# Kernel tuning notes

Hardware: AMD Instinct MI355X
Metric: run time of the kernel (lower is better)

The kernel has to match this reference:

```python
import jax, jax.numpy as jnp
import numpy as np

B, N, E = 128, 2000, 2000
EMBED, HIDDEN = 256, 512


def setup_inputs() -> dict:
    key = jax.random.key(0)
    k1, k2, k3, k4, k5, k6, k7 = jax.random.split(key, 7)
    node_embeddings = jax.random.normal(k1, (B, N, EMBED), dtype=jnp.float32)
    locs = jax.random.uniform(k2, (B, N, 2), dtype=jnp.float32)
    edge_list = jax.random.randint(k3, (B, E, 2), 0, N, dtype=jnp.int64)
    in_dim = 2 * EMBED + 1
    # Kaiming-ish init for the two Linear layers of edge_scorer
    W1 = jax.random.normal(k4, (in_dim, HIDDEN), dtype=jnp.float32) / np.sqrt(in_dim)
    b1 = jnp.zeros((HIDDEN,), dtype=jnp.float32)
    W2 = jax.random.normal(k5, (HIDDEN, 1), dtype=jnp.float32) / np.sqrt(HIDDEN)
    b2 = jnp.zeros((1,), dtype=jnp.float32)
    return {
        "node_embeddings": node_embeddings,
        "locs": locs,
        "edge_list": edge_list,
        "delete_bias": 0,
        "W1": W1,
        "b1": b1,
        "W2": W2,
        "b2": b2,
    }


def reference(node_embeddings, locs, edge_list, delete_bias, W1, b1, W2, b2):
    # valid mask for -1-padded edges
    valid = (edge_list[..., 0] >= 0) & (edge_list[..., 1] >= 0)  # (B, E)
    edges = jnp.clip(edge_list, 0, None)
    bidx = jnp.arange(node_embeddings.shape[0])[:, None]  # (B, 1)
    i, j = edges[..., 0], edges[..., 1]  # (B, E)
    emb_i = node_embeddings[bidx, i]  # (B, E, D)
    emb_j = node_embeddings[bidx, j]  # (B, E, D)
    d = locs[bidx, i] - locs[bidx, j]  # (B, E, 2)
    dist = jnp.sqrt(jnp.sum(d * d, axis=-1, keepdims=True))  # (B, E, 1)
    feats = jnp.concatenate([emb_i, emb_j, dist], axis=-1)  # (B, E, 2D+1)
    h = jax.nn.relu(jnp.einsum('bef,fh->beh', feats, W1) + b1)
    logits = (jnp.einsum('beh,ho->beo', h, W2) + b2)[..., 0]  # (B, E)
    logits = jnp.where(valid, logits, -jnp.inf)
    return logits + jnp.float32(delete_bias)
```

## Files before the change

### kernel.cpp

```cpp
#include <hip/hip_runtime.h>
#include <math.h>

#define EMBED    256
#define HIDDEN   512
#define KDIM     512
#define Nn       2000
#define Ee       2000
#define BM       64
#define NTHREADS 512
#define NBLK     4000
#define PITCH    72

typedef __attribute__((ext_vector_type(8)))  short bf16x8;
typedef __attribute__((ext_vector_type(16))) float f32x16;

static __device__ __forceinline__ short f2bf(float f) {
  unsigned u = __builtin_bit_cast(unsigned, f);
  u += 0x7fffu + ((u >> 16) & 1u);
  return (short)(u >> 16);
}

static __device__ __forceinline__ bf16x8 cvt8(float4 a, float4 b) {
  bf16x8 v;
  v[0]=f2bf(a.x); v[1]=f2bf(a.y); v[2]=f2bf(a.z); v[3]=f2bf(a.w);
  v[4]=f2bf(b.x); v[5]=f2bf(b.y); v[6]=f2bf(b.z); v[7]=f2bf(b.w);
  return v;
}

__global__ void w1f_kernel(const float* __restrict__ W1, short* __restrict__ W1F) {
  const int t  = blockIdx.x * 512 + threadIdx.x;
  const int l  = t & 63;
  const int tk = (t >> 6) & 31;
  const int tn = t >> 11;
  const int n  = tn * 32 + (l & 31);
  const int k0 = tk * 16 + (l >> 5) * 8;
  bf16x8 v;
#pragma unroll
  for (int q = 0; q < 8; ++q)
    v[q] = f2bf(W1[(size_t)(k0 + q) * HIDDEN + n]);
  *(bf16x8*)(W1F + (size_t)t * 8) = v;
}

__global__ __launch_bounds__(NTHREADS, 4)
void edge_kernel(const float* __restrict__ emb, const float* __restrict__ locs,
                 const int* __restrict__ edges, const int* __restrict__ dbias,
                 const float* __restrict__ W1, const float* __restrict__ b1,
                 const float* __restrict__ W2, const float* __restrict__ b2,
                 const short* __restrict__ W1F, float* __restrict__ out)
{
  __shared__ short  feat[2][BM][PITCH];
  __shared__ float4 ep_s[HIDDEN];
  __shared__ float  part_s[8][BM];
  __shared__ float  dist_s[BM];
  __shared__ int    valid_s[BM];
  __shared__ int    ibase_s[BM];
  __shared__ int    jbase_s[BM];

  const int tid = threadIdx.x;

  const int wg = (blockIdx.x & 7) * (NBLK / 8) + (blockIdx.x >> 3);

  if (tid < BM) {
    const int g  = wg * BM + tid;
    const int b  = g / Ee;
    const int i0 = edges[2 * g];
    const int j0 = edges[2 * g + 1];
    valid_s[tid] = (i0 >= 0) && (j0 >= 0);
    const int ib = b * Nn + (i0 < 0 ? 0 : i0);
    const int jb = b * Nn + (j0 < 0 ? 0 : j0);
    ibase_s[tid] = ib;
    jbase_s[tid] = jb;
    const float dx = locs[2 * (size_t)ib]     - locs[2 * (size_t)jb];
    const float dy = locs[2 * (size_t)ib + 1] - locs[2 * (size_t)jb + 1];
    dist_s[tid] = sqrtf(dx * dx + dy * dy);
  }
  ep_s[tid] = make_float4(b1[tid], W1[(size_t)KDIM * HIDDEN + tid], W2[tid], 0.f);
  asm volatile("s_waitcnt lgkmcnt(0)" ::: "memory");
  __builtin_amdgcn_s_barrier();
  asm volatile("" ::: "memory");

  const int e  = tid >> 3;
  const int sq = tid & 7;

  const int lane = tid & 63;
  const int ng   = tid >> 6;
  const int ln31 = lane & 31;
  const int kg   = lane >> 5;

  {
    const float* p = emb + (size_t)ibase_s[e] * EMBED + sq * 8;
    float4 v0 = *(const float4*)(p);
    float4 v1 = *(const float4*)(p + 4);
    *(bf16x8*)&feat[0][e][sq * 8] = cvt8(v0, v1);
  }
  float4 gh0, gh1;
  {
    const float* p = emb + (size_t)ibase_s[e] * EMBED + 64 + sq * 8;
    gh0 = *(const float4*)(p);
    gh1 = *(const float4*)(p + 4);
  }
  asm volatile("s_waitcnt lgkmcnt(0)" ::: "memory");
  __builtin_amdgcn_s_barrier();
  asm volatile("" ::: "memory");

  f32x16 acc[2][2];
#pragma unroll
  for (int et = 0; et < 2; ++et)
#pragma unroll
    for (int nt = 0; nt < 2; ++nt)
#pragma unroll
      for (int q = 0; q < 16; ++q) acc[et][nt][q] = 0.f;

#pragma unroll 1
  for (int c = 0; c < 8; ++c) {
    const int bb = c & 1;
    const int nb = bb ^ 1;

    const short* wb = W1F + ((size_t)(ng * 2) * 32 + c * 4) * 512 + lane * 8;
    bf16x8 wa0[4], wa1[4];
#pragma unroll
    for (int ks = 0; ks < 4; ++ks) {
      wa0[ks] = *(const bf16x8*)(wb + ks * 512);
      wa1[ks] = *(const bf16x8*)(wb + 32 * 512 + ks * 512);
    }
#pragma unroll
    for (int ks = 0; ks < 4; ++ks) {
      bf16x8 fb0 = *(const bf16x8*)(&feat[bb][ln31][ks * 16 + kg * 8]);
      bf16x8 fb1 = *(const bf16x8*)(&feat[bb][32 + ln31][ks * 16 + kg * 8]);
      acc[0][0] = __builtin_amdgcn_mfma_f32_32x32x16_bf16(wa0[ks], fb0, acc[0][0], 0, 0, 0);
      acc[0][1] = __builtin_amdgcn_mfma_f32_32x32x16_bf16(wa1[ks], fb0, acc[0][1], 0, 0, 0);
      acc[1][0] = __builtin_amdgcn_mfma_f32_32x32x16_bf16(wa0[ks], fb1, acc[1][0], 0, 0, 0);
      acc[1][1] = __builtin_amdgcn_mfma_f32_32x32x16_bf16(wa1[ks], fb1, acc[1][1], 0, 0, 0);
    }

    if (c < 7)
      *(bf16x8*)&feat[nb][e][sq * 8] = cvt8(gh0, gh1);

    __builtin_amdgcn_sched_barrier(0);
    if (c < 6) {
      const int cc = c + 2;
      const int rb = (cc < 4) ? ibase_s[e] : jbase_s[e];
      const float* p = emb + (size_t)rb * EMBED + (cc & 3) * 64 + sq * 8;
      gh0 = *(const float4*)(p);
      gh1 = *(const float4*)(p + 4);
    }
    __builtin_amdgcn_sched_barrier(0);

    asm volatile("s_waitcnt lgkmcnt(0)" ::: "memory");
    __builtin_amdgcn_s_barrier();
    asm volatile("" ::: "memory");
  }

  const float d0 = dist_s[ln31];
  const float d1 = dist_s[32 + ln31];
  float ps0 = 0.f, ps1 = 0.f;
#pragma unroll
  for (int nt = 0; nt < 2; ++nt) {
#pragma unroll
    for (int r = 0; r < 16; ++r) {
      const int n = ng * 64 + nt * 32 + (r & 3) + ((r >> 2) << 3) + (kg << 2);
      const float4 ep = ep_s[n];
      float p0 = acc[0][nt][r] + ep.x + d0 * ep.y;
      float p1 = acc[1][nt][r] + ep.x + d1 * ep.y;
      ps0 += fmaxf(p0, 0.f) * ep.z;
      ps1 += fmaxf(p1, 0.f) * ep.z;
    }
  }
  ps0 += __shfl_xor(ps0, 32, 64);
  ps1 += __shfl_xor(ps1, 32, 64);
  if (lane < 32) {
    part_s[ng][ln31]      = ps0;
    part_s[ng][32 + ln31] = ps1;
  }
  __syncthreads();

  if (tid < BM) {
    float s = 0.f;
#pragma unroll
    for (int w = 0; w < 8; ++w) s += part_s[w][tid];
    float logit = s + b2[0] + (float)dbias[0];
    if (!valid_s[tid]) logit = -__builtin_inff();
    out[(size_t)wg * BM + tid] = logit;
  }
}

extern "C" void kernel_launch(void* const* d_in, const int* in_sizes, int n_in,
                              void* d_out, int out_size, void* d_ws, size_t ws_size,
                              hipStream_t stream) {
  const float* emb   = (const float*)d_in[0];
  const float* locs  = (const float*)d_in[1];
  const int*   edges = (const int*)d_in[2];
  const int*   dbias = (const int*)d_in[3];
  const float* W1    = (const float*)d_in[4];
  const float* b1    = (const float*)d_in[5];
  const float* W2    = (const float*)d_in[6];
  const float* b2    = (const float*)d_in[7];
  float*       out   = (float*)d_out;
  short*       W1F   = (short*)d_ws;

  w1f_kernel<<<dim3(64), dim3(512), 0, stream>>>(W1, W1F);
  edge_kernel<<<dim3(NBLK), dim3(NTHREADS), 0, stream>>>(
      emb, locs, edges, dbias, W1, b1, W2, b2, (const short*)W1F, out);
}
```

Measured before the change: 164.7 us.

## Double edge tile to 128 per block and prefetch W1 fragments across chunks

```diff
diff --git a/kernel.cpp b/kernel.cpp
--- a/kernel.cpp
+++ b/kernel.cpp
@@ -6,9 +6,9 @@
 #define KDIM     512
 #define Nn       2000
 #define Ee       2000
-#define BM       64
+#define BM       128
 #define NTHREADS 512
-#define NBLK     4000
+#define NBLK     2000
 #define PITCH    72
 
 typedef __attribute__((ext_vector_type(8)))  short bf16x8;
@@ -41,7 +41,7 @@
   *(bf16x8*)(W1F + (size_t)t * 8) = v;
 }
 
-__global__ __launch_bounds__(NTHREADS, 4)
+__global__ __launch_bounds__(NTHREADS, 2)
 void edge_kernel(const float* __restrict__ emb, const float* __restrict__ locs,
                  const int* __restrict__ edges, const int* __restrict__ dbias,
                  const float* __restrict__ W1, const float* __restrict__ b1,
@@ -79,8 +79,8 @@
   __builtin_amdgcn_s_barrier();
   asm volatile("" ::: "memory");
 
-  const int e  = tid >> 3;
-  const int sq = tid & 7;
+  const int e  = tid >> 2;
+  const int sq = tid & 3;
 
   const int lane = tid & 63;
   const int ng   = tid >> 6;
@@ -88,24 +88,38 @@
   const int kg   = lane >> 5;
 
   {
-    const float* p = emb + (size_t)ibase_s[e] * EMBED + sq * 8;
+    const float* p = emb + (size_t)ibase_s[e] * EMBED + sq * 16;
     float4 v0 = *(const float4*)(p);
     float4 v1 = *(const float4*)(p + 4);
-    *(bf16x8*)&feat[0][e][sq * 8] = cvt8(v0, v1);
-  }
-  float4 gh0, gh1;
+    float4 v2 = *(const float4*)(p + 8);
+    float4 v3 = *(const float4*)(p + 12);
+    *(bf16x8*)&feat[0][e][sq * 16]     = cvt8(v0, v1);
+    *(bf16x8*)&feat[0][e][sq * 16 + 8] = cvt8(v2, v3);
+  }
+  bf16x8 wc0[4], wc1[4];
   {
-    const float* p = emb + (size_t)ibase_s[e] * EMBED + 64 + sq * 8;
-    gh0 = *(const float4*)(p);
-    gh1 = *(const float4*)(p + 4);
+    const short* wb = W1F + (size_t)(ng * 64) * 512 + lane * 8;
+#pragma unroll
+    for (int ks = 0; ks < 4; ++ks) {
+      wc0[ks] = *(const bf16x8*)(wb + ks * 512);
+      wc1[ks] = *(const bf16x8*)(wb + 32 * 512 + ks * 512);
+    }
+  }
+  float4 g0, g1, g2, g3;
+  {
+    const float* p = emb + (size_t)ibase_s[e] * EMBED + 64 + sq * 16;
+    g0 = *(const float4*)(p);
+    g1 = *(const float4*)(p + 4);
+    g2 = *(const float4*)(p + 8);
+    g3 = *(const float4*)(p + 12);
   }
   asm volatile("s_waitcnt lgkmcnt(0)" ::: "memory");
   __builtin_amdgcn_s_barrier();
   asm volatile("" ::: "memory");
 
-  f32x16 acc[2][2];
-#pragma unroll
-  for (int et = 0; et < 2; ++et)
+  f32x16 acc[4][2];
+#pragma unroll
+  for (int et = 0; et < 4; ++et)
 #pragma unroll
     for (int nt = 0; nt < 2; ++nt)
 #pragma unroll
@@ -114,63 +128,77 @@
 #pragma unroll 1
   for (int c = 0; c < 8; ++c) {
     const int bb = c & 1;
-    const int nb = bb ^ 1;
-
-    const short* wb = W1F + ((size_t)(ng * 2) * 32 + c * 4) * 512 + lane * 8;
-    bf16x8 wa0[4], wa1[4];
+    const int nbuf = bb ^ 1;
+
+    bf16x8 wn0[4], wn1[4];
+    if (c < 7) {
+      const short* wb = W1F + (size_t)(ng * 64 + (c + 1) * 4) * 512 + lane * 8;
+#pragma unroll
+      for (int ks = 0; ks < 4; ++ks) {
+        wn0[ks] = *(const bf16x8*)(wb + ks * 512);
+        wn1[ks] = *(const bf16x8*)(wb + 32 * 512 + ks * 512);
+      }
+    }
+
 #pragma unroll
     for (int ks = 0; ks < 4; ++ks) {
-      wa0[ks] = *(const bf16x8*)(wb + ks * 512);
-      wa1[ks] = *(const bf16x8*)(wb + 32 * 512 + ks * 512);
-    }
-#pragma unroll
-    for (int ks = 0; ks < 4; ++ks) {
-      bf16x8 fb0 = *(const bf16x8*)(&feat[bb][ln31][ks * 16 + kg * 8]);
-      bf16x8 fb1 = *(const bf16x8*)(&feat[bb][32 + ln31][ks * 16 + kg * 8]);
-      acc[0][0] = __builtin_amdgcn_mfma_f32_32x32x16_bf16(wa0[ks], fb0, acc[0][0], 0, 0, 0);
-      acc[0][1] = __builtin_amdgcn_mfma_f32_32x32x16_bf16(wa1[ks], fb0, acc[0][1], 0, 0, 0);
-      acc[1][0] = __builtin_amdgcn_mfma_f32_32x32x16_bf16(wa0[ks], fb1, acc[1][0], 0, 0, 0);
-      acc[1][1] = __builtin_amdgcn_mfma_f32_32x32x16_bf16(wa1[ks], fb1, acc[1][1], 0, 0, 0);
-    }
-
-    if (c < 7)
-      *(bf16x8*)&feat[nb][e][sq * 8] = cvt8(gh0, gh1);
+#pragma unroll
+      for (int et = 0; et < 4; ++et) {
+        bf16x8 fb = *(const bf16x8*)(&feat[bb][et * 32 + ln31][ks * 16 + kg * 8]);
+        acc[et][0] = __builtin_amdgcn_mfma_f32_32x32x16_bf16(wc0[ks], fb, acc[et][0], 0, 0, 0);
+        acc[et][1] = __builtin_amdgcn_mfma_f32_32x32x16_bf16(wc1[ks], fb, acc[et][1], 0, 0, 0);
+      }
+    }
+
+    if (c < 7) {
+      *(bf16x8*)&feat[nbuf][e][sq * 16]     = cvt8(g0, g1);
+      *(bf16x8*)&feat[nbuf][e][sq * 16 + 8] = cvt8(g2, g3);
+    }
 
     __builtin_amdgcn_sched_barrier(0);
     if (c < 6) {
       const int cc = c + 2;
       const int rb = (cc < 4) ? ibase_s[e] : jbase_s[e];
-      const float* p = emb + (size_t)rb * EMBED + (cc & 3) * 64 + sq * 8;
-      gh0 = *(const float4*)(p);
-      gh1 = *(const float4*)(p + 4);
+      const float* p = emb + (size_t)rb * EMBED + (cc & 3) * 64 + sq * 16;
+      g0 = *(const float4*)(p);
+      g1 = *(const float4*)(p + 4);
+      g2 = *(const float4*)(p + 8);
+      g3 = *(const float4*)(p + 12);
     }
     __builtin_amdgcn_sched_barrier(0);
 
     asm volatile("s_waitcnt lgkmcnt(0)" ::: "memory");
     __builtin_amdgcn_s_barrier();
     asm volatile("" ::: "memory");
-  }
-
-  const float d0 = dist_s[ln31];
-  const float d1 = dist_s[32 + ln31];
-  float ps0 = 0.f, ps1 = 0.f;
+
+#pragma unroll
+    for (int ks = 0; ks < 4; ++ks) { wc0[ks] = wn0[ks]; wc1[ks] = wn1[ks]; }
+  }
+
+  float dv[4], ps[4];
+#pragma unroll
+  for (int et = 0; et < 4; ++et) {
+    dv[et] = dist_s[et * 32 + ln31];
+    ps[et] = 0.f;
+  }
 #pragma unroll
   for (int nt = 0; nt < 2; ++nt) {
 #pragma unroll
     for (int r = 0; r < 16; ++r) {
       const int n = ng * 64 + nt * 32 + (r & 3) + ((r >> 2) << 3) + (kg << 2);
       const float4 ep = ep_s[n];
-      float p0 = acc[0][nt][r] + ep.x + d0 * ep.y;
-      float p1 = acc[1][nt][r] + ep.x + d1 * ep.y;
-      ps0 += fmaxf(p0, 0.f) * ep.z;
-      ps1 += fmaxf(p1, 0.f) * ep.z;
-    }
-  }
-  ps0 += __shfl_xor(ps0, 32, 64);
-  ps1 += __shfl_xor(ps1, 32, 64);
+#pragma unroll
+      for (int et = 0; et < 4; ++et) {
+        float p = acc[et][nt][r] + ep.x + dv[et] * ep.y;
+        ps[et] += fmaxf(p, 0.f) * ep.z;
+      }
+    }
+  }
+#pragma unroll
+  for (int et = 0; et < 4; ++et) ps[et] += __shfl_xor(ps[et], 32, 64);
   if (lane < 32) {
-    part_s[ng][ln31]      = ps0;
-    part_s[ng][32 + ln31] = ps1;
+#pragma unroll
+    for (int et = 0; et < 4; ++et) part_s[ng][et * 32 + ln31] = ps[et];
   }
   __syncthreads();
 
```

Result: no change. 163.4 us (-0.8%).
